# Kernel tuning notes

Measured on AMD Instinct MI355X. Metric: run time of the kernel, lower is better.

Reference implementation:

```python
import jax, jax.numpy as jnp
import numpy as np

N_EMBD = 1024
N_HEAD = 16
B, L = 4, 2048


def setup_inputs() -> dict:
    key = jax.random.key(0)
    ks = jax.random.split(key, 5)
    scale = 1.0 / np.sqrt(N_EMBD)
    x = jax.random.normal(ks[0], (B, L, N_EMBD), dtype=jnp.float32)
    # nn.Linear(n_embd, n_embd, bias=False) weights, stored torch-style (out, in)
    Wq = jax.random.uniform(ks[1], (N_EMBD, N_EMBD), jnp.float32, -scale, scale)
    Wk = jax.random.uniform(ks[2], (N_EMBD, N_EMBD), jnp.float32, -scale, scale)
    Wv = jax.random.uniform(ks[3], (N_EMBD, N_EMBD), jnp.float32, -scale, scale)
    Wp = jax.random.uniform(ks[4], (N_EMBD, N_EMBD), jnp.float32, -scale, scale)
    attn_mask = jnp.ones((B, L), dtype=jnp.int32)
    return {"x": x, "Wq": Wq, "Wk": Wk, "Wv": Wv, "Wp": Wp, "attn_mask": attn_mask}


def reference(x, Wq, Wk, Wv, Wp, attn_mask):
    Bq, Lq, C = x.shape
    hd = C // N_HEAD
    # torch Linear: y = x @ W.T
    def split_heads(y):
        return y.reshape(Bq, Lq, N_HEAD, hd).transpose(0, 2, 1, 3)  # (B,H,L,hd)
    q = split_heads(x @ Wq.T)
    k = split_heads(x @ Wk.T)
    v = split_heads(x @ Wv.T)
    att = jnp.einsum("bhqd,bhkd->bhqk", q, k) / np.sqrt(hd)  # (B,H,L,L)
    causal = jnp.tril(jnp.ones((Lq, Lq), dtype=bool))
    neg_inf = jnp.float32(-jnp.inf)
    att = jnp.where(causal[None, None, :, :], att, neg_inf)
    pad = (attn_mask != 0)[:, None, None, :]  # (B,1,1,L) key-side padding mask
    att = jnp.where(pad, att, neg_inf)
    att = jax.nn.softmax(att, axis=-1)
    y = jnp.einsum("bhqk,bhkd->bhqd", att, v)
    y = y.transpose(0, 2, 1, 3).reshape(Bq, Lq, C)
    return y @ Wp.T
```

## Files before the change

kernel.cpp:

```cpp
#include <hip/hip_runtime.h>

typedef __attribute__((ext_vector_type(8))) short short8;
typedef __attribute__((ext_vector_type(4))) float floatx4;

#define CEMB 1024
#define NHEAD 16
#define HD 64
#define BATCH 4
#define SEQ 2048

#define BARRIER() asm volatile("s_waitcnt lgkmcnt(0)\n\ts_barrier" ::: "memory")

__device__ __forceinline__ unsigned short f2bf(float f) {
    union { float f; unsigned int i; } x; x.f = f;
    unsigned int r = x.i + 0x7FFFu + ((x.i >> 16) & 1u);
    return (unsigned short)(r >> 16);
}
__device__ __forceinline__ unsigned int packbf_trunc(float a, float b) {
    union { float f; unsigned int u; } x, y; x.f = a; y.f = b;
    return (x.u >> 16) | (y.u & 0xFFFF0000u);
}

#define GLD16(gp, lp) \
    __builtin_amdgcn_global_load_lds((const __attribute__((address_space(1))) void*)(gp), \
                                     (__attribute__((address_space(3))) void*)(lp), 16, 0, 0)

__global__ void cast_x(const float* __restrict__ src, unsigned short* __restrict__ dst, int n4) {
    int i = blockIdx.x * blockDim.x + threadIdx.x;
    if (i < n4) {
        float4 v = ((const float4*)src)[i];
        ushort4 o;
        o.x = f2bf(v.x); o.y = f2bf(v.y); o.z = f2bf(v.z); o.w = f2bf(v.w);
        ((ushort4*)dst)[i] = o;
    }
}

__global__ void cast_w(const float* __restrict__ w0, const float* __restrict__ w1,
                       const float* __restrict__ w2, const float* __restrict__ w3,
                       unsigned short* __restrict__ o0, unsigned short* __restrict__ o1,
                       unsigned short* __restrict__ o2, unsigned short* __restrict__ o3) {
    int which = blockIdx.y;
    const float* src = which == 0 ? w0 : which == 1 ? w1 : which == 2 ? w2 : w3;
    unsigned short* dst = which == 0 ? o0 : which == 1 ? o1 : which == 2 ? o2 : o3;
    float scale = (which == 0) ? 0.125f : 1.0f;
    int i = blockIdx.x * blockDim.x + threadIdx.x;
    float4 v = ((const float4*)src)[i];
    ushort4 o;
    o.x = f2bf(v.x * scale); o.y = f2bf(v.y * scale);
    o.z = f2bf(v.z * scale); o.w = f2bf(v.w * scale);
    ((ushort4*)dst)[i] = o;
}


#define PHASE(Ab, Bb, mh, nh) do {                                              \
    short8 af[4][2], bfr[2][2];                                                 \
    _Pragma("unroll")                                                           \
    for (int mm = 0; mm < 4; ++mm) {                                            \
        af[mm][0] = *(const short8*)((Ab) + aOffR + (mh)*4096 + mm*1024 + ck0); \
        af[mm][1] = *(const short8*)((Ab) + aOffR + (mh)*4096 + mm*1024 + ck1); \
    }                                                                           \
    _Pragma("unroll")                                                           \
    for (int nn = 0; nn < 2; ++nn) {                                            \
        bfr[nn][0] = *(const short8*)((Bb) + bOffR + (nh)*2048 + nn*1024 + ck0);\
        bfr[nn][1] = *(const short8*)((Bb) + bOffR + (nh)*2048 + nn*1024 + ck1);\
    }                                                                           \
    __builtin_amdgcn_s_setprio(1);                                              \
    _Pragma("unroll")                                                           \
    for (int mm = 0; mm < 4; ++mm)                                              \
        _Pragma("unroll")                                                       \
        for (int nn = 0; nn < 2; ++nn) {                                        \
            acc[(mh)*4+mm][(nh)*2+nn] = __builtin_amdgcn_mfma_f32_16x16x32_bf16(\
                af[mm][0], bfr[nn][0], acc[(mh)*4+mm][(nh)*2+nn], 0, 0, 0);     \
            acc[(mh)*4+mm][(nh)*2+nn] = __builtin_amdgcn_mfma_f32_16x16x32_bf16(\
                af[mm][1], bfr[nn][1], acc[(mh)*4+mm][(nh)*2+nn], 0, 0, 0);     \
        }                                                                       \
    __builtin_amdgcn_s_setprio(0);                                              \
    __builtin_amdgcn_sched_barrier(0);                                          \
} while (0)

#define STAGE(Ab, Bb, k0) do {                                                  \
    GLD16(aS + (k0),              (Ab) + aL);                                   \
    GLD16(aS + (k0) +  8 * CEMB,  (Ab) + aL + 512);                             \
    GLD16(aS + (k0) + 16 * CEMB,  (Ab) + aL + 1024);                            \
    GLD16(aS + (k0) + 24 * CEMB,  (Ab) + aL + 1536);                            \
    GLD16(bS + (k0),              (Bb) + aL);                                   \
    GLD16(bS + (k0) +  8 * CEMB,  (Bb) + aL + 512);                             \
    GLD16(bS + (k0) + 16 * CEMB,  (Bb) + aL + 1024);                            \
    GLD16(bS + (k0) + 24 * CEMB,  (Bb) + aL + 1536);                            \
} while (0)

#define PHASE4(Ab, Bb, t, do_stage) do {                                        \
    short8 af[4][2], bfr[2][2];                                                 \
    _Pragma("unroll")                                                           \
    for (int mm = 0; mm < 4; ++mm) {                                            \
        af[mm][0] = *(const short8*)((Ab) + aOffR + 4096 + mm*1024 + ck0);      \
        af[mm][1] = *(const short8*)((Ab) + aOffR + 4096 + mm*1024 + ck1);      \
    }                                                                           \
    _Pragma("unroll")                                                           \
    for (int nn = 0; nn < 2; ++nn) {                                            \
        bfr[nn][0] = *(const short8*)((Bb) + bOffR + 2048 + nn*1024 + ck0);     \
        bfr[nn][1] = *(const short8*)((Bb) + bOffR + 2048 + nn*1024 + ck1);     \
    }                                                                           \
    asm volatile("s_waitcnt lgkmcnt(0)\n\ts_barrier" ::: "memory");             \
    __builtin_amdgcn_sched_barrier(0);                                          \
    if (do_stage) STAGE(Ab, Bb, ((t) + 2) * 64);                                \
    __builtin_amdgcn_s_setprio(1);                                              \
    _Pragma("unroll")                                                           \
    for (int mm = 0; mm < 4; ++mm)                                              \
        _Pragma("unroll")                                                       \
        for (int nn = 0; nn < 2; ++nn) {                                        \
            acc[4+mm][2+nn] = __builtin_amdgcn_mfma_f32_16x16x32_bf16(          \
                af[mm][0], bfr[nn][0], acc[4+mm][2+nn], 0, 0, 0);               \
            acc[4+mm][2+nn] = __builtin_amdgcn_mfma_f32_16x16x32_bf16(          \
                af[mm][1], bfr[nn][1], acc[4+mm][2+nn], 0, 0, 0);               \
        }                                                                       \
    __builtin_amdgcn_s_setprio(0);                                              \
    __builtin_amdgcn_sched_barrier(0);                                          \
} while (0)

#define TILE(t, VMN, do_stage) do {                                             \
    unsigned short* Ab = &As[(t) & 1][0];                                       \
    unsigned short* Bb = &Bs[(t) & 1][0];                                       \
    asm volatile("s_waitcnt vmcnt(" #VMN ")\n\ts_barrier" ::: "memory");        \
    PHASE(Ab, Bb, 0, 0);                                                        \
    PHASE(Ab, Bb, 1, 0);                                                        \
    PHASE(Ab, Bb, 0, 1);                                                        \
    PHASE4(Ab, Bb, t, do_stage);                                                \
} while (0)

__launch_bounds__(512, 2)
__global__ void gemm256(const unsigned short* __restrict__ A,
                        const unsigned short* __restrict__ W,
                        void* __restrict__ O0, void* __restrict__ O1,
                        void* __restrict__ O2, int mode, int ntn) {
    __shared__ unsigned short As[2][16384];
    __shared__ unsigned short Bs[2][16384];

    int nwg = gridDim.x;
    int bid = blockIdx.x;
    int wg = (bid & 7) * (nwg >> 3) + (bid >> 3);
    int mt = wg / ntn;
    int nt = wg - mt * ntn;
    int m0 = mt * 256, n0 = nt * 256;

    int tid = threadIdx.x;
    int wave = tid >> 6, lane = tid & 63;
    int l16 = lane & 15, quad = lane >> 4;
    int wm = wave >> 2, wn = wave & 3;

    int srow = lane >> 3;
    int scol = ((lane & 7) ^ srow) * 8;
    const unsigned short* aS = A + (size_t)(m0 + wave * 32 + srow) * CEMB + scol;
    const unsigned short* bS = W + (size_t)(n0 + wave * 32 + srow) * CEMB + scol;
    int aL = wave * 2048;

    int aOffR = (wm * 128 + l16) * 64;
    int bOffR = (wn * 64 + l16) * 64;
    int ck0 = (quad ^ (l16 & 7)) * 8;
    int ck1 = ck0 ^ 32;

    floatx4 acc[8][4];
    #pragma unroll
    for (int mm = 0; mm < 8; ++mm)
        #pragma unroll
        for (int nn = 0; nn < 4; ++nn) acc[mm][nn] = (floatx4){0.f, 0.f, 0.f, 0.f};

    STAGE(&As[0][0], &Bs[0][0], 0);
    STAGE(&As[1][0], &Bs[1][0], 64);

    #pragma unroll 2
    for (int t = 0; t < 14; ++t) { TILE(t, 8, true); }
    TILE(14, 8, false);
    TILE(15, 0, false);

    if (mode == 1) {
        float* Of = (float*)O0;
        #pragma unroll
        for (int mf = 0; mf < 8; ++mf)
            #pragma unroll
            for (int j = 0; j < 4; ++j) {
                int m = m0 + wm * 128 + mf * 16 + quad * 4 + j;
                #pragma unroll
                for (int nf = 0; nf < 4; ++nf) {
                    int n = n0 + wn * 64 + nf * 16 + l16;
                    Of[(size_t)m * CEMB + n] = acc[mf][nf][j];
                }
            }
    } else {
        int which = n0 >> 10;
        unsigned short* out = (unsigned short*)(which == 0 ? O0 : which == 1 ? O1 : O2);
        if (which < 2) {
            #pragma unroll
            for (int mf = 0; mf < 8; ++mf)
                #pragma unroll
                for (int j = 0; j < 4; ++j) {
                    int m = m0 + wm * 128 + mf * 16 + quad * 4 + j;
                    int bb = m >> 11, ll = m & (SEQ - 1);
                    #pragma unroll
                    for (int nf = 0; nf < 4; ++nf) {
                        int n = (n0 & (CEMB - 1)) + wn * 64 + nf * 16 + l16;
                        int h = n >> 6, d = n & (HD - 1);
                        out[(size_t)((bb * NHEAD + h) * SEQ + ll) * HD + d] =
                            f2bf(acc[mf][nf][j]);
                    }
                }
        } else {
            #pragma unroll
            for (int mf = 0; mf < 8; ++mf) {
                int m = m0 + wm * 128 + mf * 16 + quad * 4;
                int bb = m >> 11, ll = m & (SEQ - 1);
                #pragma unroll
                for (int nf = 0; nf < 4; ++nf) {
                    int n = (n0 & (CEMB - 1)) + wn * 64 + nf * 16 + l16;
                    int h = n >> 6, d = n & (HD - 1);
                    ushort4 o4;
                    o4.x = f2bf(acc[mf][nf][0]); o4.y = f2bf(acc[mf][nf][1]);
                    o4.z = f2bf(acc[mf][nf][2]); o4.w = f2bf(acc[mf][nf][3]);
                    *(ushort4*)&out[(size_t)((bb * NHEAD + h) * HD + d) * SEQ + ll] = o4;
                }
            }
        }
    }
}

__launch_bounds__(256, 2)
__global__ void attn_mfma(const unsigned short* __restrict__ Qb,
                          const unsigned short* __restrict__ Kb,
                          const unsigned short* __restrict__ Vtg,
                          const int* __restrict__ amask,
                          unsigned short* __restrict__ Yb) {
    __shared__ unsigned short Ks[64 * 64];
    __shared__ unsigned short Vs[64 * 64];
    __shared__ unsigned short Ps[128 * 64];

    int tid = threadIdx.x;
    int wave = tid >> 6;
    int lane = tid & 63;
    int l16 = lane & 15;
    int quad = lane >> 4;
    int l7 = l16 & 7;
    int pair = blockIdx.x;
    int bh = blockIdx.y;
    int bidx = bh >> 4;
    int h = bh & (NHEAD - 1);
    size_t hbase = (size_t)bh * SEQ * HD;

    int r0 = tid >> 3, p0 = tid & 7;
    int cl = p0 ^ (r0 & 7);
    unsigned short* kDst0 = Ks + r0 * 64 + p0 * 8;
    unsigned short* kDst1 = kDst0 + 32 * 64;
    unsigned short* vDst0 = Vs + r0 * 64 + p0 * 8;
    unsigned short* vDst1 = vDst0 + 32 * 64;
    const unsigned short* kSrc0 = Kb + hbase + (size_t)r0 * HD + cl * 8;
    const unsigned short* kSrc1 = kSrc0 + (size_t)32 * HD;
    const unsigned short* vSrc0 = Vtg + hbase + (size_t)r0 * SEQ + cl * 8;
    const unsigned short* vSrc1 = vSrc0 + (size_t)32 * SEQ;
    const int* mSrc = amask + bidx * SEQ + quad * 4;

    #pragma unroll
    for (int pass = 0; pass < 2; ++pass) {
        int qt = pass == 0 ? (15 - pair) : pair;
        int q0 = qt * 128;
        int nkt = 2 * qt + 2;

        short8 qf[2][2];
        #pragma unroll
        for (int qsub = 0; qsub < 2; ++qsub)
            #pragma unroll
            for (int kk = 0; kk < 2; ++kk)
                qf[qsub][kk] = *(const short8*)(Qb + hbase +
                    (size_t)(q0 + wave * 32 + qsub * 16 + l16) * HD + kk * 32 + quad * 8);

        short8 kr0 = *(const short8*)(kSrc0);
        short8 kr1 = *(const short8*)(kSrc1);
        short8 vr0 = *(const short8*)(vSrc0);
        short8 vr1 = *(const short8*)(vSrc1);
        int4 cmi[4];
        #pragma unroll
        for (int t = 0; t < 4; ++t) cmi[t] = *(const int4*)(mSrc + t * 16);

        floatx4 o[2][4];
        #pragma unroll
        for (int qsub = 0; qsub < 2; ++qsub)
            #pragma unroll
            for (int t = 0; t < 4; ++t) o[qsub][t] = (floatx4){0.f, 0.f, 0.f, 0.f};
        float ls[2] = {0.f, 0.f};

        int qw = q0 + wave * 32;

        for (int jt = 0; jt < nkt; ++jt) {
            BARRIER();
            *(short8*)kDst0 = kr0;
            *(short8*)kDst1 = kr1;
            *(short8*)vDst0 = vr0;
            *(short8*)vDst1 = vr1;
            int4 cm[4];
            #pragma unroll
            for (int t = 0; t < 4; ++t) cm[t] = cmi[t];
            if (jt + 1 < nkt) {
                size_t ko = (size_t)(jt + 1) * 64;
                kr0 = *(const short8*)(kSrc0 + ko * HD);
                kr1 = *(const short8*)(kSrc1 + ko * HD);
                vr0 = *(const short8*)(vSrc0 + ko);
                vr1 = *(const short8*)(vSrc1 + ko);
                #pragma unroll
                for (int t = 0; t < 4; ++t) cmi[t] = *(const int4*)(mSrc + (jt + 1) * 64 + t * 16);
            }
            BARRIER();

            if (jt * 64 <= qw + 31) {
                floatx4 sc[2][4];
                #pragma unroll
                for (int qsub = 0; qsub < 2; ++qsub)
                    #pragma unroll
                    for (int t = 0; t < 4; ++t) sc[qsub][t] = (floatx4){0.f, 0.f, 0.f, 0.f};
                #pragma unroll
                for (int kk = 0; kk < 2; ++kk)
                    #pragma unroll
                    for (int t = 0; t < 4; ++t) {
                        short8 aK = *(const short8*)(Ks + (t * 16 + l16) * 64 +
                                                     ((kk * 4 + quad) ^ l7) * 8);
                        #pragma unroll
                        for (int qsub = 0; qsub < 2; ++qsub)
                            sc[qsub][t] = __builtin_amdgcn_mfma_f32_16x16x32_bf16(
                                aK, qf[qsub][kk], sc[qsub][t], 0, 0, 0);
                    }

                bool needc = (jt * 64 + 63 > qw);

                #pragma unroll
                for (int qsub = 0; qsub < 2; ++qsub) {
                    int qi = q0 + wave * 32 + qsub * 16 + l16;
                    #pragma unroll
                    for (int t = 0; t < 4; ++t) {
                        int kb = jt * 64 + t * 16 + quad * 4;
                        float p[4];
                        #pragma unroll
                        for (int j = 0; j < 4; ++j) {
                            float sv = sc[qsub][t][j];
                            if (needc) sv = (kb + j <= qi) ? sv : -1e30f;
                            sv = cm[t][j] ? sv : -1e30f;
                            p[j] = __expf(sv);
                            ls[qsub] += p[j];
                        }
                        int row = wave * 32 + qsub * 16 + l16;
                        int pos = (t * 2 + (quad >> 1)) ^ l7;
                        uint2 pk;
                        pk.x = packbf_trunc(p[0], p[1]);
                        pk.y = packbf_trunc(p[2], p[3]);
                        *(uint2*)(Ps + row * 64 + pos * 8 + (quad & 1) * 4) = pk;
                    }
                }

                #pragma unroll
                for (int kk = 0; kk < 2; ++kk) {
                    short8 pa[2];
                    #pragma unroll
                    for (int qsub = 0; qsub < 2; ++qsub)
                        pa[qsub] = *(const short8*)(Ps + (wave * 32 + qsub * 16 + l16) * 64 +
                                                    ((kk * 4 + quad) ^ l7) * 8);
                    #pragma unroll
                    for (int t = 0; t < 4; ++t) {
                        short8 vb = *(const short8*)(Vs + (t * 16 + l16) * 64 +
                                                     ((kk * 4 + quad) ^ l7) * 8);
                        #pragma unroll
                        for (int qsub = 0; qsub < 2; ++qsub)
                            o[qsub][t] = __builtin_amdgcn_mfma_f32_16x16x32_bf16(
                                pa[qsub], vb, o[qsub][t], 0, 0, 0);
                    }
                }
            }
        }

        #pragma unroll
        for (int qsub = 0; qsub < 2; ++qsub) {
            ls[qsub] += __shfl_xor(ls[qsub], 16, 64);
            ls[qsub] += __shfl_xor(ls[qsub], 32, 64);
        }

        #pragma unroll
        for (int qsub = 0; qsub < 2; ++qsub)
            #pragma unroll
            for (int j = 0; j < 4; ++j) {
                float lq = __shfl(ls[qsub], quad * 4 + j, 64);
                float inv = 1.0f / lq;
                size_t row = (size_t)bidx * SEQ + q0 + wave * 32 + qsub * 16 + quad * 4 + j;
                #pragma unroll
                for (int t = 0; t < 4; ++t)
                    Yb[row * CEMB + h * HD + t * 16 + l16] = f2bf(o[qsub][t][j] * inv);
            }
    }
}

extern "C" void kernel_launch(void* const* d_in, const int* in_sizes, int n_in,
                              void* d_out, int out_size, void* d_ws, size_t ws_size,
                              hipStream_t stream) {
    const float* x  = (const float*)d_in[0];
    const float* Wq = (const float*)d_in[1];
    const float* Wk = (const float*)d_in[2];
    const float* Wv = (const float*)d_in[3];
    const float* Wp = (const float*)d_in[4];
    const int* amask = (const int*)d_in[5];

    char* ws = (char*)d_ws;
    unsigned short* xb  = (unsigned short*)(ws + 0);
    unsigned short* Wqb = (unsigned short*)(ws + (16u << 20));
    unsigned short* Wkb = (unsigned short*)(ws + (18u << 20));
    unsigned short* Wvb = (unsigned short*)(ws + (20u << 20));
    unsigned short* Wpb = (unsigned short*)(ws + (22u << 20));
    unsigned short* Qb  = (unsigned short*)(ws + (24u << 20));
    unsigned short* Kb  = (unsigned short*)(ws + (40u << 20));
    unsigned short* Vtg = (unsigned short*)(ws + (56u << 20));
    unsigned short* Yb  = (unsigned short*)(ws + (72u << 20));

    const int NX4 = (BATCH * SEQ * CEMB) / 4;
    const int NW4 = (CEMB * CEMB) / 4;
    cast_x<<<dim3(NX4 / 256), 256, 0, stream>>>(x, xb, NX4);
    cast_w<<<dim3(NW4 / 256, 4), 256, 0, stream>>>(Wq, Wk, Wv, Wp, Wqb, Wkb, Wvb, Wpb);

    gemm256<<<dim3(32 * 12), 512, 0, stream>>>(
        xb, Wqb, (void*)Qb, (void*)Kb, (void*)Vtg, 0, 12);

    attn_mfma<<<dim3(8, BATCH * NHEAD), 256, 0, stream>>>(Qb, Kb, Vtg, amask, Yb);

    gemm256<<<dim3(32 * 4), 512, 0, stream>>>(
        Yb, Wpb, d_out, nullptr, nullptr, 1, 4);
}
```

Measured before the change: 278.4 us.

## Shrink GEMM tile to 128x256 and flatten attention grid with causal-balanced ordering

The GEMM kernel now uses a 128x256 block tile with smaller A staging, so it launches twice as many workgroups for better CU occupancy. The barrier and waitcnt placement inside each phase is also reworked. The attention kernel drops its two-pass pairing of query tiles for a 1D grid of 1024 single-tile blocks, ordered so causal work is balanced, and raises launch bounds to 4. The log2(e) factor is folded into the Wq scale so exp2f can replace __expf, at the cost of more blocks and smaller per-block reuse.

```diff
diff --git a/kernel.cpp b/kernel.cpp
--- a/kernel.cpp
+++ b/kernel.cpp
@@ -42,7 +42,7 @@
     int which = blockIdx.y;
     const float* src = which == 0 ? w0 : which == 1 ? w1 : which == 2 ? w2 : w3;
     unsigned short* dst = which == 0 ? o0 : which == 1 ? o1 : which == 2 ? o2 : o3;
-    float scale = (which == 0) ? 0.125f : 1.0f;
+    float scale = (which == 0) ? 0.125f * 1.44269504088896f : 1.0f;
     int i = blockIdx.x * blockDim.x + threadIdx.x;
     float4 v = ((const float4*)src)[i];
     ushort4 o;
@@ -52,88 +52,92 @@
 }
 
 
-#define PHASE(Ab, Bb, mh, nh) do {                                              \
-    short8 af[4][2], bfr[2][2];                                                 \
-    _Pragma("unroll")                                                           \
-    for (int mm = 0; mm < 4; ++mm) {                                            \
-        af[mm][0] = *(const short8*)((Ab) + aOffR + (mh)*4096 + mm*1024 + ck0); \
-        af[mm][1] = *(const short8*)((Ab) + aOffR + (mh)*4096 + mm*1024 + ck1); \
+#define MFMA __builtin_amdgcn_mfma_f32_16x16x32_bf16
+
+#define PH(Ab, Bb, mh, nh) do {                                                 \
+    short8 af[2][2], bf_[2][2];                                                 \
+    _Pragma("unroll")                                                           \
+    for (int mm = 0; mm < 2; ++mm) {                                            \
+        af[mm][0] = *(const short8*)((Ab) + aOffR + ((mh)*2+mm)*1024 + ck0);    \
+        af[mm][1] = *(const short8*)((Ab) + aOffR + ((mh)*2+mm)*1024 + ck1);    \
     }                                                                           \
     _Pragma("unroll")                                                           \
     for (int nn = 0; nn < 2; ++nn) {                                            \
-        bfr[nn][0] = *(const short8*)((Bb) + bOffR + (nh)*2048 + nn*1024 + ck0);\
-        bfr[nn][1] = *(const short8*)((Bb) + bOffR + (nh)*2048 + nn*1024 + ck1);\
+        bf_[nn][0] = *(const short8*)((Bb) + bOffR + ((nh)*2+nn)*1024 + ck0);   \
+        bf_[nn][1] = *(const short8*)((Bb) + bOffR + ((nh)*2+nn)*1024 + ck1);   \
     }                                                                           \
+    asm volatile("s_barrier" ::: "memory");                                     \
+    asm volatile("s_waitcnt lgkmcnt(0)" ::: "memory");                          \
+    __builtin_amdgcn_sched_barrier(0);                                          \
     __builtin_amdgcn_s_setprio(1);                                              \
     _Pragma("unroll")                                                           \
-    for (int mm = 0; mm < 4; ++mm)                                              \
+    for (int mm = 0; mm < 2; ++mm)                                              \
         _Pragma("unroll")                                                       \
         for (int nn = 0; nn < 2; ++nn) {                                        \
-            acc[(mh)*4+mm][(nh)*2+nn] = __builtin_amdgcn_mfma_f32_16x16x32_bf16(\
-                af[mm][0], bfr[nn][0], acc[(mh)*4+mm][(nh)*2+nn], 0, 0, 0);     \
-            acc[(mh)*4+mm][(nh)*2+nn] = __builtin_amdgcn_mfma_f32_16x16x32_bf16(\
-                af[mm][1], bfr[nn][1], acc[(mh)*4+mm][(nh)*2+nn], 0, 0, 0);     \
+            acc[(mh)*2+mm][(nh)*2+nn] = MFMA(af[mm][0], bf_[nn][0],             \
+                                             acc[(mh)*2+mm][(nh)*2+nn], 0,0,0); \
+            acc[(mh)*2+mm][(nh)*2+nn] = MFMA(af[mm][1], bf_[nn][1],             \
+                                             acc[(mh)*2+mm][(nh)*2+nn], 0,0,0); \
+        }                                                                       \
+    __builtin_amdgcn_s_setprio(0);                                              \
+    __builtin_amdgcn_sched_barrier(0);                                          \
+    asm volatile("s_barrier" ::: "memory");                                     \
+} while (0)
+
+#define STAGE(Ab, Bb, k0) do {                                                  \
+    GLD16(aS + (k0),             (Ab) + aLA);                                   \
+    GLD16(aS + (k0) +  8 * CEMB, (Ab) + aLA + 512);                             \
+    GLD16(bS + (k0),             (Bb) + aLB);                                   \
+    GLD16(bS + (k0) +  8 * CEMB, (Bb) + aLB + 512);                             \
+    GLD16(bS + (k0) + 16 * CEMB, (Bb) + aLB + 1024);                            \
+    GLD16(bS + (k0) + 24 * CEMB, (Bb) + aLB + 1536);                            \
+} while (0)
+
+#define PH3(Ab, Bb, t, do_stage) do {                                           \
+    short8 af[2][2], bf_[2][2];                                                 \
+    _Pragma("unroll")                                                           \
+    for (int mm = 0; mm < 2; ++mm) {                                            \
+        af[mm][0] = *(const short8*)((Ab) + aOffR + (2+mm)*1024 + ck0);         \
+        af[mm][1] = *(const short8*)((Ab) + aOffR + (2+mm)*1024 + ck1);         \
+    }                                                                           \
+    _Pragma("unroll")                                                           \
+    for (int nn = 0; nn < 2; ++nn) {                                            \
+        bf_[nn][0] = *(const short8*)((Bb) + bOffR + (2+nn)*1024 + ck0);        \
+        bf_[nn][1] = *(const short8*)((Bb) + bOffR + (2+nn)*1024 + ck1);        \
+    }                                                                           \
+    asm volatile("s_waitcnt lgkmcnt(0)" ::: "memory");                          \
+    __builtin_amdgcn_sched_barrier(0);                                          \
+    asm volatile("s_barrier" ::: "memory");                                     \
+    if (do_stage) STAGE(Ab, Bb, ((t) + 2) * 64);                                \
+    __builtin_amdgcn_s_setprio(1);                                              \
+    _Pragma("unroll")                                                           \
+    for (int mm = 0; mm < 2; ++mm)                                              \
+        _Pragma("unroll")                                                       \
+        for (int nn = 0; nn < 2; ++nn) {                                        \
+            acc[2+mm][2+nn] = MFMA(af[mm][0], bf_[nn][0], acc[2+mm][2+nn],0,0,0);\
+            acc[2+mm][2+nn] = MFMA(af[mm][1], bf_[nn][1], acc[2+mm][2+nn],0,0,0);\
         }                                                                       \
     __builtin_amdgcn_s_setprio(0);                                              \
     __builtin_amdgcn_sched_barrier(0);                                          \
 } while (0)
 
-#define STAGE(Ab, Bb, k0) do {                                                  \
-    GLD16(aS + (k0),              (Ab) + aL);                                   \
-    GLD16(aS + (k0) +  8 * CEMB,  (Ab) + aL + 512);                             \
-    GLD16(aS + (k0) + 16 * CEMB,  (Ab) + aL + 1024);                            \
-    GLD16(aS + (k0) + 24 * CEMB,  (Ab) + aL + 1536);                            \
-    GLD16(bS + (k0),              (Bb) + aL);                                   \
-    GLD16(bS + (k0) +  8 * CEMB,  (Bb) + aL + 512);                             \
-    GLD16(bS + (k0) + 16 * CEMB,  (Bb) + aL + 1024);                            \
-    GLD16(bS + (k0) + 24 * CEMB,  (Bb) + aL + 1536);                            \
-} while (0)
-
-#define PHASE4(Ab, Bb, t, do_stage) do {                                        \
-    short8 af[4][2], bfr[2][2];                                                 \
-    _Pragma("unroll")                                                           \
-    for (int mm = 0; mm < 4; ++mm) {                                            \
-        af[mm][0] = *(const short8*)((Ab) + aOffR + 4096 + mm*1024 + ck0);      \
-        af[mm][1] = *(const short8*)((Ab) + aOffR + 4096 + mm*1024 + ck1);      \
-    }                                                                           \
-    _Pragma("unroll")                                                           \
-    for (int nn = 0; nn < 2; ++nn) {                                            \
-        bfr[nn][0] = *(const short8*)((Bb) + bOffR + 2048 + nn*1024 + ck0);     \
-        bfr[nn][1] = *(const short8*)((Bb) + bOffR + 2048 + nn*1024 + ck1);     \
-    }                                                                           \
-    asm volatile("s_waitcnt lgkmcnt(0)\n\ts_barrier" ::: "memory");             \
-    __builtin_amdgcn_sched_barrier(0);                                          \
-    if (do_stage) STAGE(Ab, Bb, ((t) + 2) * 64);                                \
-    __builtin_amdgcn_s_setprio(1);                                              \
-    _Pragma("unroll")                                                           \
-    for (int mm = 0; mm < 4; ++mm)                                              \
-        _Pragma("unroll")                                                       \
-        for (int nn = 0; nn < 2; ++nn) {                                        \
-            acc[4+mm][2+nn] = __builtin_amdgcn_mfma_f32_16x16x32_bf16(          \
-                af[mm][0], bfr[nn][0], acc[4+mm][2+nn], 0, 0, 0);               \
-            acc[4+mm][2+nn] = __builtin_amdgcn_mfma_f32_16x16x32_bf16(          \
-                af[mm][1], bfr[nn][1], acc[4+mm][2+nn], 0, 0, 0);               \
-        }                                                                       \
-    __builtin_amdgcn_s_setprio(0);                                              \
-    __builtin_amdgcn_sched_barrier(0);                                          \
-} while (0)
-
 #define TILE(t, VMN, do_stage) do {                                             \
     unsigned short* Ab = &As[(t) & 1][0];                                       \
     unsigned short* Bb = &Bs[(t) & 1][0];                                       \
-    asm volatile("s_waitcnt vmcnt(" #VMN ")\n\ts_barrier" ::: "memory");        \
-    PHASE(Ab, Bb, 0, 0);                                                        \
-    PHASE(Ab, Bb, 1, 0);                                                        \
-    PHASE(Ab, Bb, 0, 1);                                                        \
-    PHASE4(Ab, Bb, t, do_stage);                                                \
+    asm volatile("s_waitcnt vmcnt(" #VMN ")" ::: "memory");                     \
+    asm volatile("s_barrier" ::: "memory");                                     \
+    PH(Ab, Bb, 0, 0);                                                           \
+    PH(Ab, Bb, 1, 0);                                                           \
+    PH(Ab, Bb, 0, 1);                                                           \
+    PH3(Ab, Bb, t, do_stage);                                                   \
 } while (0)
 
 __launch_bounds__(512, 2)
-__global__ void gemm256(const unsigned short* __restrict__ A,
+__global__ void gemm_8p(const unsigned short* __restrict__ A,
                         const unsigned short* __restrict__ W,
                         void* __restrict__ O0, void* __restrict__ O1,
                         void* __restrict__ O2, int mode, int ntn) {
-    __shared__ unsigned short As[2][16384];
+    __shared__ unsigned short As[2][8192];
     __shared__ unsigned short Bs[2][16384];
 
     int nwg = gridDim.x;
@@ -141,7 +145,7 @@
     int wg = (bid & 7) * (nwg >> 3) + (bid >> 3);
     int mt = wg / ntn;
     int nt = wg - mt * ntn;
-    int m0 = mt * 256, n0 = nt * 256;
+    int m0 = mt * 128, n0 = nt * 256;
 
     int tid = threadIdx.x;
     int wave = tid >> 6, lane = tid & 63;
@@ -150,36 +154,40 @@
 
     int srow = lane >> 3;
     int scol = ((lane & 7) ^ srow) * 8;
-    const unsigned short* aS = A + (size_t)(m0 + wave * 32 + srow) * CEMB + scol;
+    const unsigned short* aS = A + (size_t)(m0 + wave * 16 + srow) * CEMB + scol;
     const unsigned short* bS = W + (size_t)(n0 + wave * 32 + srow) * CEMB + scol;
-    int aL = wave * 2048;
-
-    int aOffR = (wm * 128 + l16) * 64;
+    int aLA = wave * 1024;
+    int aLB = wave * 2048;
+
+    int aOffR = (wm * 64 + l16) * 64;
     int bOffR = (wn * 64 + l16) * 64;
     int ck0 = (quad ^ (l16 & 7)) * 8;
     int ck1 = ck0 ^ 32;
 
-    floatx4 acc[8][4];
-    #pragma unroll
-    for (int mm = 0; mm < 8; ++mm)
+    floatx4 acc[4][4];
+    #pragma unroll
+    for (int mm = 0; mm < 4; ++mm)
         #pragma unroll
         for (int nn = 0; nn < 4; ++nn) acc[mm][nn] = (floatx4){0.f, 0.f, 0.f, 0.f};
 
     STAGE(&As[0][0], &Bs[0][0], 0);
     STAGE(&As[1][0], &Bs[1][0], 64);
 
-    #pragma unroll 2
-    for (int t = 0; t < 14; ++t) { TILE(t, 8, true); }
-    TILE(14, 8, false);
+    for (int tt = 0; tt < 7; ++tt) {
+        int t = 2 * tt;
+        TILE(t, 6, true);
+        TILE(t + 1, 6, true);
+    }
+    TILE(14, 6, false);
     TILE(15, 0, false);
 
     if (mode == 1) {
         float* Of = (float*)O0;
         #pragma unroll
-        for (int mf = 0; mf < 8; ++mf)
+        for (int mf = 0; mf < 4; ++mf)
             #pragma unroll
             for (int j = 0; j < 4; ++j) {
-                int m = m0 + wm * 128 + mf * 16 + quad * 4 + j;
+                int m = m0 + wm * 64 + mf * 16 + quad * 4 + j;
                 #pragma unroll
                 for (int nf = 0; nf < 4; ++nf) {
                     int n = n0 + wn * 64 + nf * 16 + l16;
@@ -191,10 +199,10 @@
         unsigned short* out = (unsigned short*)(which == 0 ? O0 : which == 1 ? O1 : O2);
         if (which < 2) {
             #pragma unroll
-            for (int mf = 0; mf < 8; ++mf)
+            for (int mf = 0; mf < 4; ++mf)
                 #pragma unroll
                 for (int j = 0; j < 4; ++j) {
-                    int m = m0 + wm * 128 + mf * 16 + quad * 4 + j;
+                    int m = m0 + wm * 64 + mf * 16 + quad * 4 + j;
                     int bb = m >> 11, ll = m & (SEQ - 1);
                     #pragma unroll
                     for (int nf = 0; nf < 4; ++nf) {
@@ -206,8 +214,8 @@
                 }
         } else {
             #pragma unroll
-            for (int mf = 0; mf < 8; ++mf) {
-                int m = m0 + wm * 128 + mf * 16 + quad * 4;
+            for (int mf = 0; mf < 4; ++mf) {
+                int m = m0 + wm * 64 + mf * 16 + quad * 4;
                 int bb = m >> 11, ll = m & (SEQ - 1);
                 #pragma unroll
                 for (int nf = 0; nf < 4; ++nf) {
@@ -223,7 +231,7 @@
     }
 }
 
-__launch_bounds__(256, 2)
+__launch_bounds__(256, 4)
 __global__ void attn_mfma(const unsigned short* __restrict__ Qb,
                           const unsigned short* __restrict__ Kb,
                           const unsigned short* __restrict__ Vtg,
@@ -239,8 +247,17 @@
     int l16 = lane & 15;
     int quad = lane >> 4;
     int l7 = l16 & 7;
-    int pair = blockIdx.x;
-    int bh = blockIdx.y;
+
+    int n = blockIdx.x;
+    int r = n >> 8;
+    int i = n & 255;
+    int base = i & 15;
+    int bh = (i >> 4) + (r << 4);
+    int qt = (r == 0) ? base
+           : (r == 1) ? 15 - base
+           : (r == 2) ? (base ^ 8)
+                      : 15 - (base ^ 8);
+
     int bidx = bh >> 4;
     int h = bh & (NHEAD - 1);
     size_t hbase = (size_t)bh * SEQ * HD;
@@ -257,139 +274,135 @@
     const unsigned short* vSrc1 = vSrc0 + (size_t)32 * SEQ;
     const int* mSrc = amask + bidx * SEQ + quad * 4;
 
-    #pragma unroll
-    for (int pass = 0; pass < 2; ++pass) {
-        int qt = pass == 0 ? (15 - pair) : pair;
-        int q0 = qt * 128;
-        int nkt = 2 * qt + 2;
-
-        short8 qf[2][2];
-        #pragma unroll
-        for (int qsub = 0; qsub < 2; ++qsub)
+    int q0 = qt * 128;
+    int nkt = 2 * qt + 2;
+
+    short8 qf[2][2];
+    #pragma unroll
+    for (int qsub = 0; qsub < 2; ++qsub)
+        #pragma unroll
+        for (int kk = 0; kk < 2; ++kk)
+            qf[qsub][kk] = *(const short8*)(Qb + hbase +
+                (size_t)(q0 + wave * 32 + qsub * 16 + l16) * HD + kk * 32 + quad * 8);
+
+    short8 kr0 = *(const short8*)(kSrc0);
+    short8 kr1 = *(const short8*)(kSrc1);
+    short8 vr0 = *(const short8*)(vSrc0);
+    short8 vr1 = *(const short8*)(vSrc1);
+    int4 cmi[4];
+    #pragma unroll
+    for (int t = 0; t < 4; ++t) cmi[t] = *(const int4*)(mSrc + t * 16);
+
+    floatx4 o[2][4];
+    #pragma unroll
+    for (int qsub = 0; qsub < 2; ++qsub)
+        #pragma unroll
+        for (int t = 0; t < 4; ++t) o[qsub][t] = (floatx4){0.f, 0.f, 0.f, 0.f};
+    float ls[2] = {0.f, 0.f};
+
+    int qw = q0 + wave * 32;
+
+    for (int jt = 0; jt < nkt; ++jt) {
+        BARRIER();
+        *(short8*)kDst0 = kr0;
+        *(short8*)kDst1 = kr1;
+        *(short8*)vDst0 = vr0;
+        *(short8*)vDst1 = vr1;
+        int4 cm[4];
+        #pragma unroll
+        for (int t = 0; t < 4; ++t) cm[t] = cmi[t];
+        if (jt + 1 < nkt) {
+            size_t ko = (size_t)(jt + 1) * 64;
+            kr0 = *(const short8*)(kSrc0 + ko * HD);
+            kr1 = *(const short8*)(kSrc1 + ko * HD);
+            vr0 = *(const short8*)(vSrc0 + ko);
+            vr1 = *(const short8*)(vSrc1 + ko);
+            #pragma unroll
+            for (int t = 0; t < 4; ++t) cmi[t] = *(const int4*)(mSrc + (jt + 1) * 64 + t * 16);
+        }
+        BARRIER();
+
+        if (jt * 64 <= qw + 31) {
+            floatx4 sc[2][4];
+            #pragma unroll
+            for (int qsub = 0; qsub < 2; ++qsub)
+                #pragma unroll
+                for (int t = 0; t < 4; ++t) sc[qsub][t] = (floatx4){0.f, 0.f, 0.f, 0.f};
             #pragma unroll
             for (int kk = 0; kk < 2; ++kk)
-                qf[qsub][kk] = *(const short8*)(Qb + hbase +
-                    (size_t)(q0 + wave * 32 + qsub * 16 + l16) * HD + kk * 32 + quad * 8);
-
-        short8 kr0 = *(const short8*)(kSrc0);
-        short8 kr1 = *(const short8*)(kSrc1);
-        short8 vr0 = *(const short8*)(vSrc0);
-        short8 vr1 = *(const short8*)(vSrc1);
-        int4 cmi[4];
-        #pragma unroll
-        for (int t = 0; t < 4; ++t) cmi[t] = *(const int4*)(mSrc + t * 16);
-
-        floatx4 o[2][4];
-        #pragma unroll
-        for (int qsub = 0; qsub < 2; ++qsub)
-            #pragma unroll
-            for (int t = 0; t < 4; ++t) o[qsub][t] = (floatx4){0.f, 0.f, 0.f, 0.f};
-        float ls[2] = {0.f, 0.f};
-
-        int qw = q0 + wave * 32;
-
-        for (int jt = 0; jt < nkt; ++jt) {
-            BARRIER();
-            *(short8*)kDst0 = kr0;
-            *(short8*)kDst1 = kr1;
-            *(short8*)vDst0 = vr0;
-            *(short8*)vDst1 = vr1;
-            int4 cm[4];
-            #pragma unroll
-            for (int t = 0; t < 4; ++t) cm[t] = cmi[t];
-            if (jt + 1 < nkt) {
-                size_t ko = (size_t)(jt + 1) * 64;
-                kr0 = *(const short8*)(kSrc0 + ko * HD);
-                kr1 = *(const short8*)(kSrc1 + ko * HD);
-                vr0 = *(const short8*)(vSrc0 + ko);
-                vr1 = *(const short8*)(vSrc1 + ko);
-                #pragma unroll
-                for (int t = 0; t < 4; ++t) cmi[t] = *(const int4*)(mSrc + (jt + 1) * 64 + t * 16);
-            }
-            BARRIER();
-
-            if (jt * 64 <= qw + 31) {
-                floatx4 sc[2][4];
-                #pragma unroll
-                for (int qsub = 0; qsub < 2; ++qsub)
-                    #pragma unroll
-                    for (int t = 0; t < 4; ++t) sc[qsub][t] = (floatx4){0.f, 0.f, 0.f, 0.f};
-                #pragma unroll
-                for (int kk = 0; kk < 2; ++kk)
-                    #pragma unroll
-                    for (int t = 0; t < 4; ++t) {
-                        short8 aK = *(const short8*)(Ks + (t * 16 + l16) * 64 +
-                                                     ((kk * 4 + quad) ^ l7) * 8);
-                        #pragma unroll
-                        for (int qsub = 0; qsub < 2; ++qsub)
-                            sc[qsub][t] = __builtin_amdgcn_mfma_f32_16x16x32_bf16(
-                                aK, qf[qsub][kk], sc[qsub][t], 0, 0, 0);
-                    }
-
-                bool needc = (jt * 64 + 63 > qw);
-
-                #pragma unroll
-                for (int qsub = 0; qsub < 2; ++qsub) {
-                    int qi = q0 + wave * 32 + qsub * 16 + l16;
-                    #pragma unroll
-                    for (int t = 0; t < 4; ++t) {
-                        int kb = jt * 64 + t * 16 + quad * 4;
-                        float p[4];
-                        #pragma unroll
-                        for (int j = 0; j < 4; ++j) {
-                            float sv = sc[qsub][t][j];
-                            if (needc) sv = (kb + j <= qi) ? sv : -1e30f;
-                            sv = cm[t][j] ? sv : -1e30f;
-                            p[j] = __expf(sv);
-                            ls[qsub] += p[j];
-                        }
-                        int row = wave * 32 + qsub * 16 + l16;
-                        int pos = (t * 2 + (quad >> 1)) ^ l7;
-                        uint2 pk;
-                        pk.x = packbf_trunc(p[0], p[1]);
-                        pk.y = packbf_trunc(p[2], p[3]);
-                        *(uint2*)(Ps + row * 64 + pos * 8 + (quad & 1) * 4) = pk;
-                    }
-                }
-
-                #pragma unroll
-                for (int kk = 0; kk < 2; ++kk) {
-                    short8 pa[2];
+                #pragma unroll
+                for (int t = 0; t < 4; ++t) {
+                    short8 aK = *(const short8*)(Ks + (t * 16 + l16) * 64 +
+                                                 ((kk * 4 + quad) ^ l7) * 8);
                     #pragma unroll
                     for (int qsub = 0; qsub < 2; ++qsub)
-                        pa[qsub] = *(const short8*)(Ps + (wave * 32 + qsub * 16 + l16) * 64 +
-                                                    ((kk * 4 + quad) ^ l7) * 8);
+                        sc[qsub][t] = __builtin_amdgcn_mfma_f32_16x16x32_bf16(
+                            aK, qf[qsub][kk], sc[qsub][t], 0, 0, 0);
+                }
+
+            bool needc = (jt * 64 + 63 > qw);
+
+            #pragma unroll
+            for (int qsub = 0; qsub < 2; ++qsub) {
+                int qi = q0 + wave * 32 + qsub * 16 + l16;
+                #pragma unroll
+                for (int t = 0; t < 4; ++t) {
+                    int kb = jt * 64 + t * 16 + quad * 4;
+                    float p[4];
                     #pragma unroll
-                    for (int t = 0; t < 4; ++t) {
-                        short8 vb = *(const short8*)(Vs + (t * 16 + l16) * 64 +
-                                                     ((kk * 4 + quad) ^ l7) * 8);
-                        #pragma unroll
-                        for (int qsub = 0; qsub < 2; ++qsub)
-                            o[qsub][t] = __builtin_amdgcn_mfma_f32_16x16x32_bf16(
-                                pa[qsub], vb, o[qsub][t], 0, 0, 0);
+                    for (int j = 0; j < 4; ++j) {
+                        float sv = sc[qsub][t][j];
+                        if (needc) sv = (kb + j <= qi) ? sv : -1e30f;
+                        sv = cm[t][j] ? sv : -1e30f;
+                        p[j] = exp2f(sv);
+                        ls[qsub] += p[j];
                     }
+                    int row = wave * 32 + qsub * 16 + l16;
+                    int pos = (t * 2 + (quad >> 1)) ^ l7;
+                    uint2 pk;
+                    pk.x = packbf_trunc(p[0], p[1]);
+                    pk.y = packbf_trunc(p[2], p[3]);
+                    *(uint2*)(Ps + row * 64 + pos * 8 + (quad & 1) * 4) = pk;
+                }
+            }
+
+            #pragma unroll
+            for (int kk = 0; kk < 2; ++kk) {
+                short8 pa[2];
+                #pragma unroll
+                for (int qsub = 0; qsub < 2; ++qsub)
+                    pa[qsub] = *(const short8*)(Ps + (wave * 32 + qsub * 16 + l16) * 64 +
+                                                ((kk * 4 + quad) ^ l7) * 8);
+                #pragma unroll
+                for (int t = 0; t < 4; ++t) {
+                    short8 vb = *(const short8*)(Vs + (t * 16 + l16) * 64 +
+                                                 ((kk * 4 + quad) ^ l7) * 8);
+                    #pragma unroll
+                    for (int qsub = 0; qsub < 2; ++qsub)
+                        o[qsub][t] = __builtin_amdgcn_mfma_f32_16x16x32_bf16(
+                            pa[qsub], vb, o[qsub][t], 0, 0, 0);
                 }
             }
         }
-
-        #pragma unroll
-        for (int qsub = 0; qsub < 2; ++qsub) {
-            ls[qsub] += __shfl_xor(ls[qsub], 16, 64);
-            ls[qsub] += __shfl_xor(ls[qsub], 32, 64);
+    }
+
+    #pragma unroll
+    for (int qsub = 0; qsub < 2; ++qsub) {
+        ls[qsub] += __shfl_xor(ls[qsub], 16, 64);
+        ls[qsub] += __shfl_xor(ls[qsub], 32, 64);
+    }
+
+    #pragma unroll
+    for (int qsub = 0; qsub < 2; ++qsub)
+        #pragma unroll
+        for (int j = 0; j < 4; ++j) {
+            float lq = __shfl(ls[qsub], quad * 4 + j, 64);
+            float inv = 1.0f / lq;
+            size_t row = (size_t)bidx * SEQ + q0 + wave * 32 + qsub * 16 + quad * 4 + j;
+            #pragma unroll
+            for (int t = 0; t < 4; ++t)
+                Yb[row * CEMB + h * HD + t * 16 + l16] = f2bf(o[qsub][t][j] * inv);
         }
-
-        #pragma unroll
-        for (int qsub = 0; qsub < 2; ++qsub)
-            #pragma unroll
-            for (int j = 0; j < 4; ++j) {
-                float lq = __shfl(ls[qsub], quad * 4 + j, 64);
-                float inv = 1.0f / lq;
-                size_t row = (size_t)bidx * SEQ + q0 + wave * 32 + qsub * 16 + quad * 4 + j;
-                #pragma unroll
-                for (int t = 0; t < 4; ++t)
-                    Yb[row * CEMB + h * HD + t * 16 + l16] = f2bf(o[qsub][t][j] * inv);
-            }
-    }
 }
 
 extern "C" void kernel_launch(void* const* d_in, const int* in_sizes, int n_in,
@@ -418,11 +431,11 @@
     cast_x<<<dim3(NX4 / 256), 256, 0, stream>>>(x, xb, NX4);
     cast_w<<<dim3(NW4 / 256, 4), 256, 0, stream>>>(Wq, Wk, Wv, Wp, Wqb, Wkb, Wvb, Wpb);
 
-    gemm256<<<dim3(32 * 12), 512, 0, stream>>>(
+    gemm_8p<<<dim3(768), 512, 0, stream>>>(
         xb, Wqb, (void*)Qb, (void*)Kb, (void*)Vtg, 0, 12);
 
-    attn_mfma<<<dim3(8, BATCH * NHEAD), 256, 0, stream>>>(Qb, Kb, Vtg, amask, Yb);
-
-    gemm256<<<dim3(32 * 4), 512, 0, stream>>>(
+    attn_mfma<<<dim3(1024), 256, 0, stream>>>(Qb, Kb, Vtg, amask, Yb);
+
+    gemm_8p<<<dim3(256), 512, 0, stream>>>(
         Yb, Wpb, d_out, nullptr, nullptr, 1, 4);
 }
```

Result: slower. 551.7 us (+98.1%).

## Template GEMM on M tile height and fold log2e into Q scale for exp2

Applied to the files above, without the earlier changes.

The GEMM kernel becomes a template over the M tile height. The output projection now uses 128x256 tiles, which doubles its grid from 128 to 256 workgroups so more of the GPU's compute units are busy, with load counts and wait counters adjusted to match. Separately, log2(e) is folded into the Q weight scale so the attention softmax can call exp2f instead of __expf, dropping a multiply per score. Smaller tiles reduce operand reuse per workgroup.

```diff
diff --git a/kernel.cpp b/kernel.cpp
--- a/kernel.cpp
+++ b/kernel.cpp
@@ -42,7 +42,7 @@
     int which = blockIdx.y;
     const float* src = which == 0 ? w0 : which == 1 ? w1 : which == 2 ? w2 : w3;
     unsigned short* dst = which == 0 ? o0 : which == 1 ? o1 : which == 2 ? o2 : o3;
-    float scale = (which == 0) ? 0.125f : 1.0f;
+    float scale = (which == 0) ? 0.125f * 1.44269504088896f : 1.0f;
     int i = blockIdx.x * blockDim.x + threadIdx.x;
     float4 v = ((const float4*)src)[i];
     ushort4 o;
@@ -52,7 +52,9 @@
 }
 
 
-#define PHASE(Ab, Bb, mh, nh) do {                                              \
+#define MFMA __builtin_amdgcn_mfma_f32_16x16x32_bf16
+
+#define PH(Ab, Bb, mh, nh) do {                                                 \
     short8 af[4][2], bfr[2][2];                                                 \
     _Pragma("unroll")                                                           \
     for (int mm = 0; mm < 4; ++mm) {                                            \
@@ -69,32 +71,34 @@
     for (int mm = 0; mm < 4; ++mm)                                              \
         _Pragma("unroll")                                                       \
         for (int nn = 0; nn < 2; ++nn) {                                        \
-            acc[(mh)*4+mm][(nh)*2+nn] = __builtin_amdgcn_mfma_f32_16x16x32_bf16(\
-                af[mm][0], bfr[nn][0], acc[(mh)*4+mm][(nh)*2+nn], 0, 0, 0);     \
-            acc[(mh)*4+mm][(nh)*2+nn] = __builtin_amdgcn_mfma_f32_16x16x32_bf16(\
-                af[mm][1], bfr[nn][1], acc[(mh)*4+mm][(nh)*2+nn], 0, 0, 0);     \
+            acc[(mh)*4+mm][(nh)*2+nn] = MFMA(af[mm][0], bfr[nn][0],             \
+                                             acc[(mh)*4+mm][(nh)*2+nn], 0,0,0); \
+            acc[(mh)*4+mm][(nh)*2+nn] = MFMA(af[mm][1], bfr[nn][1],             \
+                                             acc[(mh)*4+mm][(nh)*2+nn], 0,0,0); \
         }                                                                       \
     __builtin_amdgcn_s_setprio(0);                                              \
     __builtin_amdgcn_sched_barrier(0);                                          \
 } while (0)
 
 #define STAGE(Ab, Bb, k0) do {                                                  \
-    GLD16(aS + (k0),              (Ab) + aL);                                   \
-    GLD16(aS + (k0) +  8 * CEMB,  (Ab) + aL + 512);                             \
-    GLD16(aS + (k0) + 16 * CEMB,  (Ab) + aL + 1024);                            \
-    GLD16(aS + (k0) + 24 * CEMB,  (Ab) + aL + 1536);                            \
-    GLD16(bS + (k0),              (Bb) + aL);                                   \
-    GLD16(bS + (k0) +  8 * CEMB,  (Bb) + aL + 512);                             \
-    GLD16(bS + (k0) + 16 * CEMB,  (Bb) + aL + 1024);                            \
-    GLD16(bS + (k0) + 24 * CEMB,  (Bb) + aL + 1536);                            \
+    GLD16(aS + (k0),             (Ab) + aLA);                                   \
+    GLD16(aS + (k0) +  8 * CEMB, (Ab) + aLA + 512);                             \
+    if constexpr (MH == 2) {                                                    \
+        GLD16(aS + (k0) + 16 * CEMB, (Ab) + aLA + 1024);                        \
+        GLD16(aS + (k0) + 24 * CEMB, (Ab) + aLA + 1536);                        \
+    }                                                                           \
+    GLD16(bS + (k0),             (Bb) + aLB);                                   \
+    GLD16(bS + (k0) +  8 * CEMB, (Bb) + aLB + 512);                             \
+    GLD16(bS + (k0) + 16 * CEMB, (Bb) + aLB + 1024);                            \
+    GLD16(bS + (k0) + 24 * CEMB, (Bb) + aLB + 1536);                            \
 } while (0)
 
-#define PHASE4(Ab, Bb, t, do_stage) do {                                        \
+#define PH4(Ab, Bb, MHL, t, do_stage) do {                                      \
     short8 af[4][2], bfr[2][2];                                                 \
     _Pragma("unroll")                                                           \
     for (int mm = 0; mm < 4; ++mm) {                                            \
-        af[mm][0] = *(const short8*)((Ab) + aOffR + 4096 + mm*1024 + ck0);      \
-        af[mm][1] = *(const short8*)((Ab) + aOffR + 4096 + mm*1024 + ck1);      \
+        af[mm][0] = *(const short8*)((Ab) + aOffR + (MHL)*4096 + mm*1024 + ck0);\
+        af[mm][1] = *(const short8*)((Ab) + aOffR + (MHL)*4096 + mm*1024 + ck1);\
     }                                                                           \
     _Pragma("unroll")                                                           \
     for (int nn = 0; nn < 2; ++nn) {                                            \
@@ -109,31 +113,38 @@
     for (int mm = 0; mm < 4; ++mm)                                              \
         _Pragma("unroll")                                                       \
         for (int nn = 0; nn < 2; ++nn) {                                        \
-            acc[4+mm][2+nn] = __builtin_amdgcn_mfma_f32_16x16x32_bf16(          \
-                af[mm][0], bfr[nn][0], acc[4+mm][2+nn], 0, 0, 0);               \
-            acc[4+mm][2+nn] = __builtin_amdgcn_mfma_f32_16x16x32_bf16(          \
-                af[mm][1], bfr[nn][1], acc[4+mm][2+nn], 0, 0, 0);               \
+            acc[(MHL)*4+mm][2+nn] = MFMA(af[mm][0], bfr[nn][0],                 \
+                                         acc[(MHL)*4+mm][2+nn], 0,0,0);         \
+            acc[(MHL)*4+mm][2+nn] = MFMA(af[mm][1], bfr[nn][1],                 \
+                                         acc[(MHL)*4+mm][2+nn], 0,0,0);         \
         }                                                                       \
     __builtin_amdgcn_s_setprio(0);                                              \
     __builtin_amdgcn_sched_barrier(0);                                          \
 } while (0)
 
-#define TILE(t, VMN, do_stage) do {                                             \
+#define TILE(t, drain, do_stage) do {                                           \
     unsigned short* Ab = &As[(t) & 1][0];                                       \
     unsigned short* Bb = &Bs[(t) & 1][0];                                       \
-    asm volatile("s_waitcnt vmcnt(" #VMN ")\n\ts_barrier" ::: "memory");        \
-    PHASE(Ab, Bb, 0, 0);                                                        \
-    PHASE(Ab, Bb, 1, 0);                                                        \
-    PHASE(Ab, Bb, 0, 1);                                                        \
-    PHASE4(Ab, Bb, t, do_stage);                                                \
+    if (drain) { asm volatile("s_waitcnt vmcnt(0)" ::: "memory"); }             \
+    else if constexpr (MH == 2) { asm volatile("s_waitcnt vmcnt(8)" ::: "memory"); } \
+    else { asm volatile("s_waitcnt vmcnt(6)" ::: "memory"); }                   \
+    asm volatile("s_barrier" ::: "memory");                                     \
+    if constexpr (MH == 2) {                                                    \
+        PH(Ab, Bb, 0, 0); PH(Ab, Bb, 1, 0); PH(Ab, Bb, 0, 1);                   \
+        PH4(Ab, Bb, 1, t, do_stage);                                            \
+    } else {                                                                    \
+        PH(Ab, Bb, 0, 0);                                                       \
+        PH4(Ab, Bb, 0, t, do_stage);                                            \
+    }                                                                           \
 } while (0)
 
+template<int MH>
 __launch_bounds__(512, 2)
-__global__ void gemm256(const unsigned short* __restrict__ A,
-                        const unsigned short* __restrict__ W,
-                        void* __restrict__ O0, void* __restrict__ O1,
-                        void* __restrict__ O2, int mode, int ntn) {
-    __shared__ unsigned short As[2][16384];
+__global__ void gemm_t(const unsigned short* __restrict__ A,
+                       const unsigned short* __restrict__ W,
+                       void* __restrict__ O0, void* __restrict__ O1,
+                       void* __restrict__ O2, int mode, int ntn) {
+    __shared__ unsigned short As[2][MH * 8192];
     __shared__ unsigned short Bs[2][16384];
 
     int nwg = gridDim.x;
@@ -141,7 +152,7 @@
     int wg = (bid & 7) * (nwg >> 3) + (bid >> 3);
     int mt = wg / ntn;
     int nt = wg - mt * ntn;
-    int m0 = mt * 256, n0 = nt * 256;
+    int m0 = mt * (MH * 128), n0 = nt * 256;
 
     int tid = threadIdx.x;
     int wave = tid >> 6, lane = tid & 63;
@@ -150,18 +161,19 @@
 
     int srow = lane >> 3;
     int scol = ((lane & 7) ^ srow) * 8;
-    const unsigned short* aS = A + (size_t)(m0 + wave * 32 + srow) * CEMB + scol;
+    const unsigned short* aS = A + (size_t)(m0 + wave * (MH * 16) + srow) * CEMB + scol;
     const unsigned short* bS = W + (size_t)(n0 + wave * 32 + srow) * CEMB + scol;
-    int aL = wave * 2048;
-
-    int aOffR = (wm * 128 + l16) * 64;
+    int aLA = wave * (MH * 1024);
+    int aLB = wave * 2048;
+
+    int aOffR = (wm * (MH * 64) + l16) * 64;
     int bOffR = (wn * 64 + l16) * 64;
     int ck0 = (quad ^ (l16 & 7)) * 8;
     int ck1 = ck0 ^ 32;
 
-    floatx4 acc[8][4];
+    floatx4 acc[MH * 4][4];
     #pragma unroll
-    for (int mm = 0; mm < 8; ++mm)
+    for (int mm = 0; mm < MH * 4; ++mm)
         #pragma unroll
         for (int nn = 0; nn < 4; ++nn) acc[mm][nn] = (floatx4){0.f, 0.f, 0.f, 0.f};
 
@@ -169,17 +181,17 @@
     STAGE(&As[1][0], &Bs[1][0], 64);
 
     #pragma unroll 2
-    for (int t = 0; t < 14; ++t) { TILE(t, 8, true); }
-    TILE(14, 8, false);
-    TILE(15, 0, false);
+    for (int t = 0; t < 14; ++t) { TILE(t, false, true); }
+    TILE(14, false, false);
+    TILE(15, true, false);
 
     if (mode == 1) {
         float* Of = (float*)O0;
         #pragma unroll
-        for (int mf = 0; mf < 8; ++mf)
+        for (int mf = 0; mf < MH * 4; ++mf)
             #pragma unroll
             for (int j = 0; j < 4; ++j) {
-                int m = m0 + wm * 128 + mf * 16 + quad * 4 + j;
+                int m = m0 + wm * (MH * 64) + mf * 16 + quad * 4 + j;
                 #pragma unroll
                 for (int nf = 0; nf < 4; ++nf) {
                     int n = n0 + wn * 64 + nf * 16 + l16;
@@ -191,10 +203,10 @@
         unsigned short* out = (unsigned short*)(which == 0 ? O0 : which == 1 ? O1 : O2);
         if (which < 2) {
             #pragma unroll
-            for (int mf = 0; mf < 8; ++mf)
+            for (int mf = 0; mf < MH * 4; ++mf)
                 #pragma unroll
                 for (int j = 0; j < 4; ++j) {
-                    int m = m0 + wm * 128 + mf * 16 + quad * 4 + j;
+                    int m = m0 + wm * (MH * 64) + mf * 16 + quad * 4 + j;
                     int bb = m >> 11, ll = m & (SEQ - 1);
                     #pragma unroll
                     for (int nf = 0; nf < 4; ++nf) {
@@ -206,8 +218,8 @@
                 }
         } else {
             #pragma unroll
-            for (int mf = 0; mf < 8; ++mf) {
-                int m = m0 + wm * 128 + mf * 16 + quad * 4;
+            for (int mf = 0; mf < MH * 4; ++mf) {
+                int m = m0 + wm * (MH * 64) + mf * 16 + quad * 4;
                 int bb = m >> 11, ll = m & (SEQ - 1);
                 #pragma unroll
                 for (int nf = 0; nf < 4; ++nf) {
@@ -340,7 +352,7 @@
                             float sv = sc[qsub][t][j];
                             if (needc) sv = (kb + j <= qi) ? sv : -1e30f;
                             sv = cm[t][j] ? sv : -1e30f;
-                            p[j] = __expf(sv);
+                            p[j] = exp2f(sv);
                             ls[qsub] += p[j];
                         }
                         int row = wave * 32 + qsub * 16 + l16;
@@ -418,11 +430,11 @@
     cast_x<<<dim3(NX4 / 256), 256, 0, stream>>>(x, xb, NX4);
     cast_w<<<dim3(NW4 / 256, 4), 256, 0, stream>>>(Wq, Wk, Wv, Wp, Wqb, Wkb, Wvb, Wpb);
 
-    gemm256<<<dim3(32 * 12), 512, 0, stream>>>(
+    gemm_t<2><<<dim3(384), 512, 0, stream>>>(
         xb, Wqb, (void*)Qb, (void*)Kb, (void*)Vtg, 0, 12);
 
     attn_mfma<<<dim3(8, BATCH * NHEAD), 256, 0, stream>>>(Qb, Kb, Vtg, amask, Yb);
 
-    gemm256<<<dim3(32 * 4), 512, 0, stream>>>(
+    gemm_t<1><<<dim3(256), 512, 0, stream>>>(
         Yb, Wpb, d_out, nullptr, nullptr, 1, 4);
 }
```

Result: no change. 279.5 us (+0.4%).
